# Optimization experiments

Measured on AMD Instinct MI355X. Metric: run time of the kernel, lower is better.

Reference implementation:

```python
import jax, jax.numpy as jnp
import numpy as np

B, C, D, E, ES, TOPK = 8, 4096, 1024, 16, 256, 4096

def setup_inputs() -> dict:
    key = jax.random.key(0)
    k1, k2, k3, k4 = jax.random.split(key, 4)
    x = jax.random.normal(k1, (B, C, D), dtype=jnp.float32)
    gate = jax.random.normal(k2, (C, E), dtype=jnp.float32) / np.sqrt(D)
    lin1_weight = jax.random.normal(k3, (D, E, ES), dtype=jnp.float32) / np.sqrt(D)
    lin2_weight = jax.random.normal(k4, (E, ES, D), dtype=jnp.float32) / np.sqrt(ES)
    return {"x": x, "gate": gate, "lin1_weight": lin1_weight, "lin2_weight": lin2_weight, "topk": TOPK}

def reference(x, gate, lin1_weight, lin2_weight, topk):
    b, c, d = x.shape
    e = gate.shape[1]
    n_tokens = b * c
    # faithful to original einsum: sum x over dmodel, elementwise-mult by gate[c, e]
    gate_out = jnp.einsum('bcd,ce->bce', x, gate)            # [b, c, e]
    gate_out = jnp.transpose(gate_out, (2, 0, 1)).reshape(e, n_tokens)
    gate_out = jax.nn.softmax(gate_out, axis=1)              # softmax over tokens per expert
    topk_values, topk_indices = jax.lax.top_k(gate_out, topk)  # [e, k]
    xf = x.reshape(n_tokens, d)
    flat_idx = topk_indices.reshape(-1)
    gathered = xf[flat_idx].reshape(e, topk, d)              # dispatch
    h = jax.nn.relu(jnp.einsum('ekd,des->eks', gathered, lin1_weight))
    out = jnp.einsum('eks,esd->ekd', h, lin2_weight)
    out = out * topk_values[..., None]                       # weight by gate probs
    z = jnp.zeros_like(xf).at[flat_idx].add(out.reshape(-1, d))  # scatter-add combine
    return z.reshape(b, c, d)
```

## Files before the change

### kernel.cpp

```cpp
#include <hip/hip_runtime.h>
#include <hip/hip_bf16.h>

#define BB 8
#define CC 4096
#define DD 1024
#define EE 16
#define ESS 256
#define KSEL 4096
#define NTOK (BB*CC)

typedef short bf16x8 __attribute__((ext_vector_type(8)));
typedef float f32x4 __attribute__((ext_vector_type(4)));

struct PickRes { unsigned tau; unsigned n_gt; unsigned n_tie; float sm; };

__device__ __forceinline__ short f2bf(float f) {
  unsigned u = __float_as_uint(f);
  u += 0x7FFFu + ((u >> 16) & 1u);
  return (short)(u >> 16);
}
__device__ __forceinline__ float bf2f(short s) {
  return __uint_as_float(((unsigned)(unsigned short)s) << 16);
}
__device__ __forceinline__ unsigned f2key(float f) {
  unsigned u = __float_as_uint(f);
  return (u & 0x80000000u) ? ~u : (u | 0x80000000u);
}

#define ASG __attribute__((address_space(1)))
#define ASL __attribute__((address_space(3)))
__device__ __forceinline__ void gl_lds16(void* l, const void* g) {
  __builtin_amdgcn_global_load_lds((ASG const unsigned*)g, (ASL unsigned*)l, 16, 0, 0);
}

__global__ void k_logits(const float* __restrict__ x, const float* __restrict__ gate,
                         float* __restrict__ logits, short* __restrict__ xb) {
  int wid = threadIdx.x >> 6, lane = threadIdx.x & 63;
  int t = blockIdx.x * 4 + wid;
  const float4* xr = reinterpret_cast<const float4*>(x + (size_t)t * DD);
  short4* xw = reinterpret_cast<short4*>(xb + (size_t)t * DD);
  float s = 0.f;
#pragma unroll
  for (int i = 0; i < 4; ++i) {
    float4 v = xr[lane + 64 * i];
    s += v.x + v.y + v.z + v.w;
    short4 p;
    p.x = f2bf(v.x); p.y = f2bf(v.y); p.z = f2bf(v.z); p.w = f2bf(v.w);
    xw[lane + 64 * i] = p;
  }
#pragma unroll
  for (int off = 32; off; off >>= 1) s += __shfl_xor(s, off);
  if (lane < EE) {
    int c = t & (CC - 1);
    logits[(size_t)lane * NTOK + t] = s * gate[c * EE + lane];
  }
}

__global__ __launch_bounds__(1024) void k_hist(const float* __restrict__ logits,
                                               unsigned* __restrict__ ghist,
                                               float* __restrict__ separt) {
  int e = blockIdx.x & 15, seg = blockIdx.x >> 4;
  const float* L = logits + (size_t)e * NTOK + seg * 4096;
  unsigned* Hh = ghist + (size_t)e * 65536;
  int tid = threadIdx.x;
  float sl = 0.f;
#pragma unroll
  for (int i = 0; i < 4; ++i) {
    float lv = L[tid + 1024 * i];
    atomicAdd(&Hh[f2key(lv) >> 16], 1u);
    sl += expf(lv);
  }
  __shared__ float red[1024];
  red[tid] = sl; __syncthreads();
  for (int s2 = 512; s2; s2 >>= 1) {
    if (tid < s2) red[tid] += red[tid + s2];
    __syncthreads();
  }
  if (tid == 0) separt[e * 8 + seg] = red[0];
}

__global__ __launch_bounds__(1024) void k_pick(const unsigned* __restrict__ ghist,
                                               const float* __restrict__ logits,
                                               const float* __restrict__ separt,
                                               PickRes* __restrict__ pres) {
  int e = blockIdx.x;
  const unsigned* Hh = ghist + (size_t)e * 65536;
  const float* L = logits + (size_t)e * NTOK;
  int tid = threadIdx.x;
  __shared__ unsigned u0[1024], u1[1024];
  __shared__ unsigned hist256[256];
  __shared__ unsigned sh_b16, sh_ngt, sh_kth;
  __shared__ unsigned sh_p24, sh_ngt2, sh_kth2;

  unsigned cs = 0;
  for (int j = 0; j < 64; ++j) cs += Hh[tid * 64 + j];
  u0[tid] = cs; __syncthreads();
  unsigned* src = u0; unsigned* dst = u1;
  for (int d2 = 1; d2 < 1024; d2 <<= 1) {
    unsigned v = src[tid] + ((tid + d2 < 1024) ? src[tid + d2] : 0u);
    dst[tid] = v; __syncthreads();
    unsigned* tmp = src; src = dst; dst = tmp;
  }
  unsigned kth0 = KSEL;
  unsigned above = (tid < 1023) ? src[tid + 1] : 0u;
  if (above < kth0 && kth0 <= src[tid]) {
    unsigned cum = above;
    for (int j = 63; j >= 0; --j) {
      unsigned h = Hh[tid * 64 + j];
      if (cum + h >= kth0) { sh_b16 = (unsigned)(tid * 64 + j); sh_ngt = cum; sh_kth = kth0 - cum; break; }
      cum += h;
    }
  }
  __syncthreads();
  unsigned p16 = sh_b16, ngt1 = sh_ngt, kth1 = sh_kth;

  if (tid < 256) hist256[tid] = 0;
  __syncthreads();
  for (int t = tid; t < NTOK; t += 1024) {
    unsigned key = f2key(L[t]);
    if ((key >> 16) == p16) atomicAdd(&hist256[(key >> 8) & 255], 1u);
  }
  __syncthreads();
  if (tid == 0) {
    unsigned cum = 0; int d = 255;
    for (; d >= 0; --d) { unsigned h = hist256[d]; if (cum + h >= kth1) break; cum += h; }
    sh_p24 = (p16 << 8) | (unsigned)d;
    sh_ngt2 = ngt1 + cum;
    sh_kth2 = kth1 - cum;
  }
  __syncthreads();
  unsigned p24 = sh_p24, ngt2 = sh_ngt2, kth2 = sh_kth2;

  if (tid < 256) hist256[tid] = 0;
  __syncthreads();
  for (int t = tid; t < NTOK; t += 1024) {
    unsigned key = f2key(L[t]);
    if ((key >> 8) == p24) atomicAdd(&hist256[key & 255], 1u);
  }
  __syncthreads();
  if (tid == 0) {
    unsigned cum = 0; int d = 255;
    for (; d >= 0; --d) { unsigned h = hist256[d]; if (cum + h >= kth2) break; cum += h; }
    unsigned tau = (p24 << 8) | (unsigned)d;
    unsigned n_gt = ngt2 + cum;
    float sm = 0.f;
    for (int j = 0; j < 8; ++j) sm += separt[e * 8 + j];
    PickRes pr; pr.tau = tau; pr.n_gt = n_gt; pr.n_tie = KSEL - n_gt; pr.sm = sm;
    pres[e] = pr;
  }
}

__global__ __launch_bounds__(1024) void k_compact(const float* __restrict__ logits,
                                                  const PickRes* __restrict__ pres,
                                                  int* __restrict__ sel_idx,
                                                  float* __restrict__ sel_val,
                                                  int* __restrict__ inv,
                                                  unsigned* __restrict__ ctrs) {
  int e = blockIdx.x & 15, seg = blockIdx.x >> 4;
  PickRes pr = pres[e];
  const float* L = logits + (size_t)e * NTOK;
  int t0 = seg * 4096;
  int tid = threadIdx.x;
#pragma unroll
  for (int i = 0; i < 4; ++i) {
    int t = t0 + tid + 1024 * i;
    float lv = L[t];
    unsigned key = f2key(lv);
    unsigned slot = 0xFFFFFFFFu;
    if (key > pr.tau) slot = atomicAdd(&ctrs[e * 2], 1u);
    else if (key == pr.tau) {
      unsigned r = atomicAdd(&ctrs[e * 2 + 1], 1u);
      if (r < pr.n_tie) slot = pr.n_gt + r;
    }
    if (slot != 0xFFFFFFFFu) {
      sel_idx[(size_t)e * KSEL + slot] = t;
      sel_val[(size_t)e * KSEL + slot] = expf(lv) / pr.sm;
      inv[(size_t)t * EE + e] = e * KSEL + (int)slot;
    }
  }
}

__global__ void k_transpose(const float* __restrict__ src, short* __restrict__ dst,
                            int R, int C) {
  __shared__ float tile[64][65];
  int c0 = blockIdx.x * 64, r0 = blockIdx.y * 64, b = blockIdx.z;
  const float* S = src + (size_t)b * R * C;
  short* Dp = dst + (size_t)b * R * C;
  int tx = threadIdx.x & 63, ty = threadIdx.x >> 6;
#pragma unroll
  for (int i = 0; i < 16; ++i) {
    int r = ty + 4 * i;
    tile[r][tx] = S[(size_t)(r0 + r) * C + c0 + tx];
  }
  __syncthreads();
#pragma unroll
  for (int i = 0; i < 16; ++i) {
    int cR = ty + 4 * i;
    Dp[(size_t)(c0 + cR) * R + r0 + tx] = f2bf(tile[tx][cR]);
  }
}

__global__ __launch_bounds__(512, 4) void k_gemm1(
    const short* __restrict__ xb, const short* __restrict__ W1T,
    const int* __restrict__ sel_idx, const float* __restrict__ sel_val,
    short* __restrict__ H) {
  int bid = blockIdx.x;
  int m0 = ((bid >> 3) & 31) * 128;
  int e = (bid & 7) + ((bid >> 8) << 3);
  __shared__ bf16x8 As8[128 * 8];
  __shared__ bf16x8 Bs8[256 * 8];
  int tid = threadIdx.x, lane = tid & 63, wid = tid >> 6;
  int wr = wid >> 2, wc = wid & 3;
  const int* idxE = sel_idx + (size_t)e * KSEL;
  f32x4 acc[4][4] = {};

  int rowA = tid >> 3, sA = tid & 7;
  int xk = rowA & 7;
  const short* aSrc0 = xb + (size_t)idxE[m0 + rowA] * DD + (sA ^ xk) * 8;
  const short* aSrc1 = xb + (size_t)idxE[m0 + rowA + 64] * DD + (sA ^ xk) * 8;
  const short* wBase = W1T + (size_t)e * ESS * DD + (size_t)rowA * DD + (sA ^ xk) * 8;

  for (int kt = 0; kt < DD / 64; ++kt) {
    int kofs = kt * 64;
    gl_lds16(&As8[tid], aSrc0 + kofs);
    gl_lds16(&As8[512 + tid], aSrc1 + kofs);
#pragma unroll
    for (int j = 0; j < 4; ++j)
      gl_lds16(&Bs8[j * 512 + tid], wBase + (size_t)(64 * j) * DD + kofs);
    __syncthreads();
    bf16x8 af[4][2];
#pragma unroll
    for (int mg = 0; mg < 4; ++mg) {
      int row = wr * 64 + mg * 16 + (lane & 15);
#pragma unroll
      for (int h = 0; h < 2; ++h) {
        int seg = h * 4 + (lane >> 4);
        af[mg][h] = As8[row * 8 + (seg ^ (row & 7))];
      }
    }
#pragma unroll
    for (int ng = 0; ng < 4; ++ng) {
      int rowb = wc * 64 + ng * 16 + (lane & 15);
      bf16x8 b0 = Bs8[rowb * 8 + (((lane >> 4) + 0) ^ (rowb & 7))];
      bf16x8 b1 = Bs8[rowb * 8 + (((lane >> 4) + 4) ^ (rowb & 7))];
#pragma unroll
      for (int mg = 0; mg < 4; ++mg) {
        acc[mg][ng] = __builtin_amdgcn_mfma_f32_16x16x32_bf16(af[mg][0], b0, acc[mg][ng], 0, 0, 0);
        acc[mg][ng] = __builtin_amdgcn_mfma_f32_16x16x32_bf16(af[mg][1], b1, acc[mg][ng], 0, 0, 0);
      }
    }
    __syncthreads();
  }
#pragma unroll
  for (int mg = 0; mg < 4; ++mg) {
#pragma unroll
    for (int r = 0; r < 4; ++r) {
      int ml = wr * 64 + mg * 16 + (lane >> 4) * 4 + r;
      float v = sel_val[(size_t)e * KSEL + m0 + ml];
#pragma unroll
      for (int ng = 0; ng < 4; ++ng) {
        float o = fmaxf(acc[mg][ng][r], 0.f) * v;
        H[((size_t)(e * KSEL + m0 + ml)) * ESS + wc * 64 + ng * 16 + (lane & 15)] = f2bf(o);
      }
    }
  }
}

template <int COMBINE>
__global__ __launch_bounds__(512, 4) void k_gemm2(
    const short* __restrict__ H, const short* __restrict__ W2T,
    const int* __restrict__ sel_idx, float* __restrict__ z, short* __restrict__ out) {
  int bid = blockIdx.x;
  int p = (bid & 7) + ((bid >> 8) << 3);
  int m0 = ((bid >> 3) & 31) * 128;
  int n0 = (p & 3) * 256;
  int e = p >> 2;
  __shared__ bf16x8 As8[128 * 8];
  __shared__ bf16x8 Bs8[256 * 8];
  int tid = threadIdx.x, lane = tid & 63, wid = tid >> 6;
  int wr = wid >> 2, wc = wid & 3;
  f32x4 acc[4][4] = {};

  int rowA = tid >> 3, sA = tid & 7;
  int xk = rowA & 7;
  const short* hBase = H + (size_t)(e * KSEL + m0 + rowA) * ESS + (sA ^ xk) * 8;
  const short* w2Base = W2T + (size_t)(e * DD + n0 + rowA) * ESS + (sA ^ xk) * 8;

  for (int kt = 0; kt < ESS / 64; ++kt) {
    int kofs = kt * 64;
    gl_lds16(&As8[tid], hBase + kofs);
    gl_lds16(&As8[512 + tid], hBase + (size_t)64 * ESS + kofs);
#pragma unroll
    for (int j = 0; j < 4; ++j)
      gl_lds16(&Bs8[j * 512 + tid], w2Base + (size_t)(64 * j) * ESS + kofs);
    __syncthreads();
    bf16x8 af[4][2];
#pragma unroll
    for (int mg = 0; mg < 4; ++mg) {
      int row = wr * 64 + mg * 16 + (lane & 15);
#pragma unroll
      for (int h = 0; h < 2; ++h) {
        int seg = h * 4 + (lane >> 4);
        af[mg][h] = As8[row * 8 + (seg ^ (row & 7))];
      }
    }
#pragma unroll
    for (int ng = 0; ng < 4; ++ng) {
      int rowb = wc * 64 + ng * 16 + (lane & 15);
      bf16x8 b0 = Bs8[rowb * 8 + (((lane >> 4) + 0) ^ (rowb & 7))];
      bf16x8 b1 = Bs8[rowb * 8 + (((lane >> 4) + 4) ^ (rowb & 7))];
#pragma unroll
      for (int mg = 0; mg < 4; ++mg) {
        acc[mg][ng] = __builtin_amdgcn_mfma_f32_16x16x32_bf16(af[mg][0], b0, acc[mg][ng], 0, 0, 0);
        acc[mg][ng] = __builtin_amdgcn_mfma_f32_16x16x32_bf16(af[mg][1], b1, acc[mg][ng], 0, 0, 0);
      }
    }
    __syncthreads();
  }
#pragma unroll
  for (int mg = 0; mg < 4; ++mg) {
#pragma unroll
    for (int r = 0; r < 4; ++r) {
      int ml = wr * 64 + mg * 16 + (lane >> 4) * 4 + r;
      if (COMBINE) {
        short* orow = out + ((size_t)(e * KSEL + m0 + ml)) * DD + n0 + wc * 64 + (lane & 15);
#pragma unroll
        for (int ng = 0; ng < 4; ++ng) orow[ng * 16] = f2bf(acc[mg][ng][r]);
      } else {
        int token = sel_idx[(size_t)e * KSEL + m0 + ml];
        float* zr = z + (size_t)token * DD + n0 + wc * 64 + (lane & 15);
#pragma unroll
        for (int ng = 0; ng < 4; ++ng) atomicAdd(zr + ng * 16, acc[mg][ng][r]);
      }
    }
  }
}

__global__ void k_combine(const short* __restrict__ out, const int* __restrict__ inv,
                          float* __restrict__ z) {
  int wid = threadIdx.x >> 6, lane = threadIdx.x & 63;
  int t = blockIdx.x * 4 + wid;
  int g[16];
  const int4* iv4 = reinterpret_cast<const int4*>(inv + (size_t)t * EE);
#pragma unroll
  for (int q = 0; q < 4; ++q) {
    int4 v = iv4[q];
    g[4 * q] = v.x; g[4 * q + 1] = v.y; g[4 * q + 2] = v.z; g[4 * q + 3] = v.w;
  }
  float acc[16] = {};
#pragma unroll
  for (int e = 0; e < EE; ++e) {
    if (g[e] < 0) continue;
    const uint4* rp = reinterpret_cast<const uint4*>(out + (size_t)g[e] * DD + lane * 16);
    uint4 v0 = rp[0], v1 = rp[1];
    const short* s0 = reinterpret_cast<const short*>(&v0);
    const short* s1 = reinterpret_cast<const short*>(&v1);
#pragma unroll
    for (int i = 0; i < 8; ++i) acc[i] += bf2f(s0[i]);
#pragma unroll
    for (int i = 0; i < 8; ++i) acc[8 + i] += bf2f(s1[i]);
  }
  float4* zw = reinterpret_cast<float4*>(z + (size_t)t * DD + lane * 16);
#pragma unroll
  for (int i = 0; i < 4; ++i) {
    float4 o; o.x = acc[4 * i]; o.y = acc[4 * i + 1]; o.z = acc[4 * i + 2]; o.w = acc[4 * i + 3];
    zw[i] = o;
  }
}

extern "C" void kernel_launch(void* const* d_in, const int* in_sizes, int n_in,
                              void* d_out, int out_size, void* d_ws, size_t ws_size,
                              hipStream_t stream) {
  (void)in_sizes; (void)n_in;
  const float* x = (const float*)d_in[0];
  const float* gate = (const float*)d_in[1];
  const float* lin1 = (const float*)d_in[2];
  const float* lin2 = (const float*)d_in[3];
  float* z = (float*)d_out;

  char* ws = (char*)d_ws;
  size_t off = 0;
  auto alloc = [&](size_t bytes) -> void* {
    off = (off + 255) & ~(size_t)255;
    void* p = ws + off;
    off += bytes;
    return p;
  };
  float* logits = (float*)alloc((size_t)EE * NTOK * 4);
  int* sidx = (int*)alloc((size_t)EE * KSEL * 4);
  float* sval = (float*)alloc((size_t)EE * KSEL * 4);
  int* inv = (int*)alloc((size_t)NTOK * EE * 4);
  short* W1T = (short*)alloc((size_t)EE * ESS * DD * 2);
  short* W2T = (short*)alloc((size_t)EE * DD * ESS * 2);
  short* H = (short*)alloc((size_t)EE * KSEL * ESS * 2);
  short* xb = (short*)alloc((size_t)NTOK * DD * 2);
  size_t out_bytes = (size_t)EE * KSEL * DD * 2;
  bool combine = (off + 256 + out_bytes) <= ws_size;
  short* outbuf = combine ? (short*)alloc(out_bytes) : nullptr;

  unsigned* ghist = (unsigned*)H;
  float* separt = (float*)((char*)H + (size_t)EE * 65536 * 4);
  PickRes* pres = (PickRes*)((char*)separt + 1024);
  unsigned* ctrs = (unsigned*)((char*)pres + 1024);

  k_transpose<<<dim3(64, 16, 1), 256, 0, stream>>>(lin1, W1T, DD, EE * ESS);
  k_transpose<<<dim3(16, 4, 16), 256, 0, stream>>>(lin2, W2T, ESS, DD);
  k_logits<<<NTOK / 4, 256, 0, stream>>>(x, gate, logits, xb);
  hipMemsetAsync(inv, 0xFF, (size_t)NTOK * EE * 4, stream);
  hipMemsetAsync(ghist, 0, (size_t)EE * 65536 * 4, stream);
  hipMemsetAsync(ctrs, 0, 128, stream);
  k_hist<<<128, 1024, 0, stream>>>(logits, ghist, separt);
  k_pick<<<EE, 1024, 0, stream>>>(ghist, logits, separt, pres);
  k_compact<<<128, 1024, 0, stream>>>(logits, pres, sidx, sval, inv, ctrs);
  k_gemm1<<<512, 512, 0, stream>>>(xb, W1T, sidx, sval, H);
  if (combine) {
    k_gemm2<1><<<2048, 512, 0, stream>>>(H, W2T, sidx, z, outbuf);
    k_combine<<<NTOK / 4, 256, 0, stream>>>(outbuf, inv, z);
  } else {
    hipMemsetAsync(d_out, 0, (size_t)out_size * sizeof(float), stream);
    k_gemm2<0><<<2048, 512, 0, stream>>>(H, W2T, sidx, z, nullptr);
  }
}
```

Baseline: 364.6 us.

## Double-buffer GEMM LDS staging and make top-k compaction deterministic via count/scan

Both expert GEMM kernels now double-buffer their LDS tiles, issuing the next k-tile's global-to-LDS loads before the current tile's MFMAs. This is meant to overlap memory latency with compute. Launch-bounds occupancy hints drop from 4 to 1 block per CU, which may allow more registers but fewer resident waves. The top-k compaction swaps global atomic counters for a count kernel, a tiny scan kernel and in-block ballot prefix sums, so slot order becomes deterministic and atomic contention goes away, at the cost of two extra launches and an extra pass over the logits. The double-buffered loop drops one barrier per iteration, which looks like a possible race where the next stage overwrites a buffer other warps are still reading.

After: 359.9 us. About the same (-1.3%).

```diff
diff --git a/kernel.cpp b/kernel.cpp
--- a/kernel.cpp
+++ b/kernel.cpp
@@ -150,26 +150,72 @@
   }
 }
 
+__global__ __launch_bounds__(1024) void k_count(const float* __restrict__ logits,
+                                                const PickRes* __restrict__ pres,
+                                                unsigned* __restrict__ cnts) {
+  int e = blockIdx.x & 15, seg = blockIdx.x >> 4;
+  PickRes pr = pres[e];
+  const float* L = logits + (size_t)e * NTOK + seg * 4096;
+  int tid = threadIdx.x;
+  unsigned pk = 0;
+#pragma unroll
+  for (int i = 0; i < 4; ++i) {
+    unsigned key = f2key(L[tid + 1024 * i]);
+    pk += (key > pr.tau) ? 0x10000u : ((key == pr.tau) ? 1u : 0u);
+  }
+  __shared__ unsigned red[1024];
+  red[tid] = pk; __syncthreads();
+  for (int s2 = 512; s2; s2 >>= 1) {
+    if (tid < s2) red[tid] += red[tid + s2];
+    __syncthreads();
+  }
+  if (tid == 0) cnts[e * 8 + seg] = red[0];
+}
+
+__global__ void k_scan(const unsigned* __restrict__ cnts, unsigned* __restrict__ bases) {
+  int e = threadIdx.x;
+  if (e < EE) {
+    unsigned gb = 0, qb = 0;
+    for (int s = 0; s < 8; ++s) {
+      unsigned c = cnts[e * 8 + s];
+      bases[e * 8 + s] = (gb << 16) | qb;
+      gb += c >> 16; qb += c & 0xFFFFu;
+    }
+  }
+}
+
 __global__ __launch_bounds__(1024) void k_compact(const float* __restrict__ logits,
                                                   const PickRes* __restrict__ pres,
+                                                  const unsigned* __restrict__ bases,
                                                   int* __restrict__ sel_idx,
                                                   float* __restrict__ sel_val,
-                                                  int* __restrict__ inv,
-                                                  unsigned* __restrict__ ctrs) {
+                                                  int* __restrict__ inv) {
   int e = blockIdx.x & 15, seg = blockIdx.x >> 4;
   PickRes pr = pres[e];
   const float* L = logits + (size_t)e * NTOK;
-  int t0 = seg * 4096;
-  int tid = threadIdx.x;
-#pragma unroll
+  unsigned b = bases[e * 8 + seg];
+  __shared__ unsigned wtg[16], wtq[16];
+  __shared__ unsigned base_g, base_q;
+  int tid = threadIdx.x, wid = tid >> 6, lane = tid & 63;
+  if (tid == 0) { base_g = b >> 16; base_q = b & 0xFFFFu; }
+  __syncthreads();
+#pragma unroll 1
   for (int i = 0; i < 4; ++i) {
-    int t = t0 + tid + 1024 * i;
+    int t = seg * 4096 + tid + 1024 * i;
     float lv = L[t];
     unsigned key = f2key(lv);
+    bool g = key > pr.tau, q = key == pr.tau;
+    unsigned long long bg = __ballot(g), bq = __ballot(q);
+    unsigned long long lm = (1ull << lane) - 1ull;
+    unsigned pg = __popcll(bg & lm), pq = __popcll(bq & lm);
+    if (lane == 63) { wtg[wid] = pg + (g ? 1u : 0u); wtq[wid] = pq + (q ? 1u : 0u); }
+    __syncthreads();
+    unsigned og = base_g, oq = base_q;
+    for (int w2 = 0; w2 < wid; ++w2) { og += wtg[w2]; oq += wtq[w2]; }
     unsigned slot = 0xFFFFFFFFu;
-    if (key > pr.tau) slot = atomicAdd(&ctrs[e * 2], 1u);
-    else if (key == pr.tau) {
-      unsigned r = atomicAdd(&ctrs[e * 2 + 1], 1u);
+    if (g) slot = og + pg;
+    else if (q) {
+      unsigned r = oq + pq;
       if (r < pr.n_tie) slot = pr.n_gt + r;
     }
     if (slot != 0xFFFFFFFFu) {
@@ -177,6 +223,14 @@
       sel_val[(size_t)e * KSEL + slot] = expf(lv) / pr.sm;
       inv[(size_t)t * EE + e] = e * KSEL + (int)slot;
     }
+    __syncthreads();
+    if (tid == 0) {
+      unsigned sg = 0, sq = 0;
+#pragma unroll
+      for (int w2 = 0; w2 < 16; ++w2) { sg += wtg[w2]; sq += wtq[w2]; }
+      base_g += sg; base_q += sq;
+    }
+    __syncthreads();
   }
 }
 
@@ -200,15 +254,15 @@
   }
 }
 
-__global__ __launch_bounds__(512, 4) void k_gemm1(
+__global__ __launch_bounds__(512, 1) void k_gemm1(
     const short* __restrict__ xb, const short* __restrict__ W1T,
     const int* __restrict__ sel_idx, const float* __restrict__ sel_val,
     short* __restrict__ H) {
   int bid = blockIdx.x;
   int m0 = ((bid >> 3) & 31) * 128;
   int e = (bid & 7) + ((bid >> 8) << 3);
-  __shared__ bf16x8 As8[128 * 8];
-  __shared__ bf16x8 Bs8[256 * 8];
+  __shared__ bf16x8 As8[2 * 128 * 8];
+  __shared__ bf16x8 Bs8[2 * 256 * 8];
   int tid = threadIdx.x, lane = tid & 63, wid = tid >> 6;
   int wr = wid >> 2, wc = wid & 3;
   const int* idxE = sel_idx + (size_t)e * KSEL;
@@ -220,14 +274,20 @@
   const short* aSrc1 = xb + (size_t)idxE[m0 + rowA + 64] * DD + (sA ^ xk) * 8;
   const short* wBase = W1T + (size_t)e * ESS * DD + (size_t)rowA * DD + (sA ^ xk) * 8;
 
+  auto stage = [&](int b, int kt) {
+    int kofs = kt * 64;
+    gl_lds16(&As8[b * 1024 + tid], aSrc0 + kofs);
+    gl_lds16(&As8[b * 1024 + 512 + tid], aSrc1 + kofs);
+#pragma unroll
+    for (int j = 0; j < 4; ++j)
+      gl_lds16(&Bs8[b * 2048 + j * 512 + tid], wBase + (size_t)(64 * j) * DD + kofs);
+  };
+
+  stage(0, 0);
+  __syncthreads();
   for (int kt = 0; kt < DD / 64; ++kt) {
-    int kofs = kt * 64;
-    gl_lds16(&As8[tid], aSrc0 + kofs);
-    gl_lds16(&As8[512 + tid], aSrc1 + kofs);
-#pragma unroll
-    for (int j = 0; j < 4; ++j)
-      gl_lds16(&Bs8[j * 512 + tid], wBase + (size_t)(64 * j) * DD + kofs);
-    __syncthreads();
+    int cur = kt & 1;
+    if (kt < DD / 64 - 1) stage(cur ^ 1, kt + 1);
     bf16x8 af[4][2];
 #pragma unroll
     for (int mg = 0; mg < 4; ++mg) {
@@ -235,14 +295,14 @@
 #pragma unroll
       for (int h = 0; h < 2; ++h) {
         int seg = h * 4 + (lane >> 4);
-        af[mg][h] = As8[row * 8 + (seg ^ (row & 7))];
+        af[mg][h] = As8[cur * 1024 + row * 8 + (seg ^ (row & 7))];
       }
     }
 #pragma unroll
     for (int ng = 0; ng < 4; ++ng) {
       int rowb = wc * 64 + ng * 16 + (lane & 15);
-      bf16x8 b0 = Bs8[rowb * 8 + (((lane >> 4) + 0) ^ (rowb & 7))];
-      bf16x8 b1 = Bs8[rowb * 8 + (((lane >> 4) + 4) ^ (rowb & 7))];
+      bf16x8 b0 = Bs8[cur * 2048 + rowb * 8 + (((lane >> 4) + 0) ^ (rowb & 7))];
+      bf16x8 b1 = Bs8[cur * 2048 + rowb * 8 + (((lane >> 4) + 4) ^ (rowb & 7))];
 #pragma unroll
       for (int mg = 0; mg < 4; ++mg) {
         acc[mg][ng] = __builtin_amdgcn_mfma_f32_16x16x32_bf16(af[mg][0], b0, acc[mg][ng], 0, 0, 0);
@@ -267,7 +327,7 @@
 }
 
 template <int COMBINE>
-__global__ __launch_bounds__(512, 4) void k_gemm2(
+__global__ __launch_bounds__(512, 1) void k_gemm2(
     const short* __restrict__ H, const short* __restrict__ W2T,
     const int* __restrict__ sel_idx, float* __restrict__ z, short* __restrict__ out) {
   int bid = blockIdx.x;
@@ -275,8 +335,8 @@
   int m0 = ((bid >> 3) & 31) * 128;
   int n0 = (p & 3) * 256;
   int e = p >> 2;
-  __shared__ bf16x8 As8[128 * 8];
-  __shared__ bf16x8 Bs8[256 * 8];
+  __shared__ bf16x8 As8[2 * 128 * 8];
+  __shared__ bf16x8 Bs8[2 * 256 * 8];
   int tid = threadIdx.x, lane = tid & 63, wid = tid >> 6;
   int wr = wid >> 2, wc = wid & 3;
   f32x4 acc[4][4] = {};
@@ -286,14 +346,20 @@
   const short* hBase = H + (size_t)(e * KSEL + m0 + rowA) * ESS + (sA ^ xk) * 8;
   const short* w2Base = W2T + (size_t)(e * DD + n0 + rowA) * ESS + (sA ^ xk) * 8;
 
+  auto stage = [&](int b, int kt) {
+    int kofs = kt * 64;
+    gl_lds16(&As8[b * 1024 + tid], hBase + kofs);
+    gl_lds16(&As8[b * 1024 + 512 + tid], hBase + (size_t)64 * ESS + kofs);
+#pragma unroll
+    for (int j = 0; j < 4; ++j)
+      gl_lds16(&Bs8[b * 2048 + j * 512 + tid], w2Base + (size_t)(64 * j) * ESS + kofs);
+  };
+
+  stage(0, 0);
+  __syncthreads();
   for (int kt = 0; kt < ESS / 64; ++kt) {
-    int kofs = kt * 64;
-    gl_lds16(&As8[tid], hBase + kofs);
-    gl_lds16(&As8[512 + tid], hBase + (size_t)64 * ESS + kofs);
-#pragma unroll
-    for (int j = 0; j < 4; ++j)
-      gl_lds16(&Bs8[j * 512 + tid], w2Base + (size_t)(64 * j) * ESS + kofs);
-    __syncthreads();
+    int cur = kt & 1;
+    if (kt < ESS / 64 - 1) stage(cur ^ 1, kt + 1);
     bf16x8 af[4][2];
 #pragma unroll
     for (int mg = 0; mg < 4; ++mg) {
@@ -301,14 +367,14 @@
 #pragma unroll
       for (int h = 0; h < 2; ++h) {
         int seg = h * 4 + (lane >> 4);
-        af[mg][h] = As8[row * 8 + (seg ^ (row & 7))];
+        af[mg][h] = As8[cur * 1024 + row * 8 + (seg ^ (row & 7))];
       }
     }
 #pragma unroll
     for (int ng = 0; ng < 4; ++ng) {
       int rowb = wc * 64 + ng * 16 + (lane & 15);
-      bf16x8 b0 = Bs8[rowb * 8 + (((lane >> 4) + 0) ^ (rowb & 7))];
-      bf16x8 b1 = Bs8[rowb * 8 + (((lane >> 4) + 4) ^ (rowb & 7))];
+      bf16x8 b0 = Bs8[cur * 2048 + rowb * 8 + (((lane >> 4) + 0) ^ (rowb & 7))];
+      bf16x8 b1 = Bs8[cur * 2048 + rowb * 8 + (((lane >> 4) + 4) ^ (rowb & 7))];
 #pragma unroll
       for (int mg = 0; mg < 4; ++mg) {
         acc[mg][ng] = __builtin_amdgcn_mfma_f32_16x16x32_bf16(af[mg][0], b0, acc[mg][ng], 0, 0, 0);
@@ -401,17 +467,19 @@
   unsigned* ghist = (unsigned*)H;
   float* separt = (float*)((char*)H + (size_t)EE * 65536 * 4);
   PickRes* pres = (PickRes*)((char*)separt + 1024);
-  unsigned* ctrs = (unsigned*)((char*)pres + 1024);
+  unsigned* cnts = (unsigned*)((char*)pres + 1024);
+  unsigned* bases = (unsigned*)((char*)cnts + 1024);
 
   k_transpose<<<dim3(64, 16, 1), 256, 0, stream>>>(lin1, W1T, DD, EE * ESS);
   k_transpose<<<dim3(16, 4, 16), 256, 0, stream>>>(lin2, W2T, ESS, DD);
   k_logits<<<NTOK / 4, 256, 0, stream>>>(x, gate, logits, xb);
   hipMemsetAsync(inv, 0xFF, (size_t)NTOK * EE * 4, stream);
   hipMemsetAsync(ghist, 0, (size_t)EE * 65536 * 4, stream);
-  hipMemsetAsync(ctrs, 0, 128, stream);
   k_hist<<<128, 1024, 0, stream>>>(logits, ghist, separt);
   k_pick<<<EE, 1024, 0, stream>>>(ghist, logits, separt, pres);
-  k_compact<<<128, 1024, 0, stream>>>(logits, pres, sidx, sval, inv, ctrs);
+  k_count<<<128, 1024, 0, stream>>>(logits, pres, cnts);
+  k_scan<<<1, 64, 0, stream>>>(cnts, bases);
+  k_compact<<<128, 1024, 0, stream>>>(logits, pres, bases, sidx, sval, inv);
   k_gemm1<<<512, 512, 0, stream>>>(xb, W1T, sidx, sval, H);
   if (combine) {
     k_gemm2<1><<<2048, 512, 0, stream>>>(H, W2T, sidx, z, outbuf);
```
